# Kernel optimization log

Hardware: AMD Instinct MI355X
Metric: run time of the kernel (lower is better)

The kernel has to match this reference:

```python
import jax, jax.numpy as jnp
import numpy as np

KERNEL = 2
STRIDE = 2
N_QUBITS = 4
N_LAYERS = 2
PI = np.float32(np.pi)
EPS = np.float32(1e-8)


def setup_inputs() -> dict:
    key = jax.random.key(0)
    k1, k2, k3, k4 = jax.random.split(key, 4)
    x = jax.random.normal(k1, (64, 3, 512, 512), dtype=jnp.float32)
    weights = jax.random.normal(k2, (N_LAYERS, N_QUBITS, 3), dtype=jnp.float32) * 0.1
    proj_w = jax.random.normal(k3, (4, N_QUBITS, 1, 1), dtype=jnp.float32) * 0.5
    proj_b = jax.random.normal(k4, (4,), dtype=jnp.float32) * 0.1
    return {"x": x, "weights": weights, "proj_w": proj_w, "proj_b": proj_b}


def _extract_patches(x):
    # x: (B, C, H, W) -> flattened 2x2 patches of grayscale image: (B, Ho, Wo, 4)
    B, C, H, W = x.shape
    Ho = (H - KERNEL) // STRIDE + 1
    Wo = (W - KERNEL) // STRIDE + 1
    x_gray = x.mean(axis=1)  # (B, H, W)
    # stride == kernel, so non-overlapping patches via reshape
    p = x_gray.reshape(B, Ho, KERNEL, Wo, KERNEL)
    p = p.transpose(0, 1, 3, 2, 4).reshape(B, Ho, Wo, KERNEL * KERNEL)
    return p


def reference(x, weights, proj_w, proj_b):
    patches = _extract_patches(x)  # (B, Ho, Wo, 4)
    # global min-max normalization (matches patches.min()/max() over whole tensor)
    pmin = patches.min()
    pmax = patches.max()
    patches = (patches - pmin) / (pmax - pmin + EPS)

    # simplified quantum simulation, fully vectorized over (B, Ho, Wo)
    encoded = jnp.sin(patches * PI)  # (B, Ho, Wo, Q)
    for layer in range(N_LAYERS):
        w = weights[layer]  # (Q, 3)
        neighbor = jnp.roll(encoded, shift=-1, axis=-1)  # encoded[(i+1)%Q]
        mixed = encoded * jnp.cos(w[:, 0]) + neighbor * jnp.sin(w[:, 1]) + w[:, 2]
        encoded = jnp.tanh(mixed)

    # (B, Ho, Wo, Q) -> (B, Q, Ho, Wo), then 1x1 conv projection
    q = encoded.transpose(0, 3, 1, 2)
    out = jnp.einsum('bqhw,oq->bohw', q, proj_w[:, :, 0, 0]) + proj_b[None, :, None, None]
    return out
```

## Files before the change

### kernel.cpp

```cpp
#include <hip/hip_runtime.h>
#include <hip/hip_fp16.h>

constexpr int BN = 64, CH = 3, HH = 512, WW = 512;
constexpr int HO = 256, WO = 256;
constexpr int HW = HH * WW;
constexpr int HOWO = HO * WO;
constexpr float EPS_F = 1e-8f;

constexpr int TPB = 256;
constexpr int GROUPS = BN * HO * (WO / 4);
constexpr int ABLOCKS = 2048;
constexpr int AT = ABLOCKS * TPB;
constexpr int AITERS = GROUPS / AT;
constexpr int CBLOCKS = GROUPS / TPB;

constexpr size_t GRAY_HALFS = (size_t)GROUPS * 16;

__device__ __forceinline__ float fast_tanh(float x) {
    float t = __builtin_amdgcn_exp2f(x * 2.8853900817779268f);
    return 1.0f - 2.0f * __builtin_amdgcn_rcpf(t + 1.0f);
}

__global__ __launch_bounds__(TPB) void k_pass1(const float* __restrict__ x,
                                               float4* __restrict__ gray4,
                                               float* __restrict__ part) {
    const int tid = blockIdx.x * TPB + threadIdx.x;
    const float c13 = 1.0f / 3.0f;
    float vmin = __int_as_float(0x7F800000);
    float vmax = __int_as_float(0xFF800000);

    #pragma unroll
    for (int it = 0; it < AITERS; ++it) {
        int grp = it * AT + tid;
        int b   = grp >> 14;
        int rem = grp & 16383;
        int ho  = rem >> 6;
        int wp  = rem & 63;
        const float* base = x + b * (CH * HW) + (2 * ho) * WW + 8 * wp;

        float row0[8], row1[8];
        #pragma unroll
        for (int c = 0; c < CH; ++c) {
            const float* pc = base + c * HW;
            float4 u0 = *(const float4*)(pc);
            float4 u1 = *(const float4*)(pc + 4);
            float4 v0 = *(const float4*)(pc + WW);
            float4 v1 = *(const float4*)(pc + WW + 4);
            float uu[8] = {u0.x, u0.y, u0.z, u0.w, u1.x, u1.y, u1.z, u1.w};
            float vv[8] = {v0.x, v0.y, v0.z, v0.w, v1.x, v1.y, v1.z, v1.w};
            if (c == 0) {
                #pragma unroll
                for (int k = 0; k < 8; ++k) { row0[k] = uu[k]; row1[k] = vv[k]; }
            } else {
                #pragma unroll
                for (int k = 0; k < 8; ++k) { row0[k] += uu[k]; row1[k] += vv[k]; }
            }
        }
        #pragma unroll
        for (int k = 0; k < 8; ++k) {
            row0[k] *= c13; row1[k] *= c13;
            vmin = fminf(vmin, fminf(row0[k], row1[k]));
            vmax = fmaxf(vmax, fmaxf(row0[k], row1[k]));
        }
        alignas(16) __half2 h2[8];
        #pragma unroll
        for (int p = 0; p < 4; ++p) {
            h2[2 * p]     = __floats2half2_rn(row0[2 * p], row0[2 * p + 1]);
            h2[2 * p + 1] = __floats2half2_rn(row1[2 * p], row1[2 * p + 1]);
        }
        gray4[(size_t)grp * 2]     = *(const float4*)&h2[0];
        gray4[(size_t)grp * 2 + 1] = *(const float4*)&h2[4];
    }

    #pragma unroll
    for (int off = 32; off > 0; off >>= 1) {
        vmin = fminf(vmin, __shfl_down(vmin, off, 64));
        vmax = fmaxf(vmax, __shfl_down(vmax, off, 64));
    }
    __shared__ float sm[8];
    int lane = threadIdx.x & 63, wid = threadIdx.x >> 6;
    if (lane == 0) { sm[wid] = vmin; sm[4 + wid] = vmax; }
    __syncthreads();
    if (threadIdx.x == 0) {
        part[2 * blockIdx.x]     = fminf(fminf(sm[0], sm[1]), fminf(sm[2], sm[3]));
        part[2 * blockIdx.x + 1] = fmaxf(fmaxf(sm[4], sm[5]), fmaxf(sm[6], sm[7]));
    }
}

__global__ __launch_bounds__(TPB) void k_reduce(const float* __restrict__ part,
                                                float* __restrict__ mm) {
    float m = __int_as_float(0x7F800000);
    float M = __int_as_float(0xFF800000);
    #pragma unroll
    for (int i = 0; i < ABLOCKS / TPB; ++i) {
        int j = i * TPB + threadIdx.x;
        m = fminf(m, part[2 * j]);
        M = fmaxf(M, part[2 * j + 1]);
    }
    #pragma unroll
    for (int off = 32; off > 0; off >>= 1) {
        m = fminf(m, __shfl_down(m, off, 64));
        M = fmaxf(M, __shfl_down(M, off, 64));
    }
    __shared__ float sm[8];
    int lane = threadIdx.x & 63, wid = threadIdx.x >> 6;
    if (lane == 0) { sm[wid] = m; sm[4 + wid] = M; }
    __syncthreads();
    if (threadIdx.x == 0) {
        mm[0] = fminf(fminf(sm[0], sm[1]), fminf(sm[2], sm[3]));
        mm[1] = fmaxf(fmaxf(sm[4], sm[5]), fmaxf(sm[6], sm[7]));
    }
}

__global__ __launch_bounds__(TPB) void k_main(const float4* __restrict__ gray4,
                                              const float* __restrict__ wts,
                                              const float* __restrict__ pw,
                                              const float* __restrict__ pb,
                                              const float* __restrict__ mm,
                                              float* __restrict__ out) {
    int grp = blockIdx.x * TPB + threadIdx.x;
    int b   = grp >> 14;
    int rem = grp & 16383;
    int ho  = rem >> 6;
    int wp  = rem & 63;

    float pmin   = mm[0];
    float sscale = 0.5f / (mm[1] - pmin + EPS_F);

    const float inv2pi = 0.15915494309189535f;
    float c0[2][4], s1[2][4], b2[2][4];
    #pragma unroll
    for (int l = 0; l < 2; ++l)
        #pragma unroll
        for (int q = 0; q < 4; ++q) {
            c0[l][q] = __builtin_amdgcn_cosf(wts[(l * 4 + q) * 3 + 0] * inv2pi);
            s1[l][q] = __builtin_amdgcn_sinf(wts[(l * 4 + q) * 3 + 1] * inv2pi);
            b2[l][q] = wts[(l * 4 + q) * 3 + 2];
        }
    float pwr[4][4], pbr[4];
    #pragma unroll
    for (int o = 0; o < 4; ++o) {
        pbr[o] = pb[o];
        #pragma unroll
        for (int q = 0; q < 4; ++q) pwr[o][q] = pw[o * 4 + q];
    }

    alignas(16) __half2 h2[8];
    *(float4*)&h2[0] = gray4[(size_t)grp * 2];
    *(float4*)&h2[4] = gray4[(size_t)grp * 2 + 1];

    float e[4][4];
    #pragma unroll
    for (int p = 0; p < 4; ++p) {
        e[p][0] = __low2float(h2[2 * p]);     e[p][1] = __high2float(h2[2 * p]);
        e[p][2] = __low2float(h2[2 * p + 1]); e[p][3] = __high2float(h2[2 * p + 1]);
    }
    #pragma unroll
    for (int p = 0; p < 4; ++p)
        #pragma unroll
        for (int q = 0; q < 4; ++q)
            e[p][q] = __builtin_amdgcn_sinf((e[p][q] - pmin) * sscale);
    #pragma unroll
    for (int l = 0; l < 2; ++l)
        #pragma unroll
        for (int p = 0; p < 4; ++p) {
            float mq[4];
            #pragma unroll
            for (int q = 0; q < 4; ++q)
                mq[q] = e[p][q] * c0[l][q] + e[p][(q + 1) & 3] * s1[l][q] + b2[l][q];
            #pragma unroll
            for (int q = 0; q < 4; ++q) e[p][q] = fast_tanh(mq[q]);
        }

    float* ob = out + b * (4 * HOWO) + ho * WO + 4 * wp;
    #pragma unroll
    for (int o = 0; o < 4; ++o) {
        float4 v;
        float* vp = &v.x;
        #pragma unroll
        for (int p = 0; p < 4; ++p) {
            float acc = pbr[o];
            #pragma unroll
            for (int q = 0; q < 4; ++q) acc += e[p][q] * pwr[o][q];
            vp[p] = acc;
        }
        *(float4*)(ob + o * HOWO) = v;
    }
}

extern "C" void kernel_launch(void* const* d_in, const int* in_sizes, int n_in,
                              void* d_out, int out_size, void* d_ws, size_t ws_size,
                              hipStream_t stream) {
    const float* x   = (const float*)d_in[0];
    const float* wts = (const float*)d_in[1];
    const float* pw  = (const float*)d_in[2];
    const float* pb  = (const float*)d_in[3];
    float* out = (float*)d_out;

    float4* gray4 = (float4*)d_ws;
    float*  part  = (float*)((char*)d_ws + GRAY_HALFS * sizeof(__half));
    float*  mm    = part + 2 * ABLOCKS;

    k_pass1 <<<ABLOCKS, TPB, 0, stream>>>(x, gray4, part);
    k_reduce<<<1,       TPB, 0, stream>>>(part, mm);
    k_main  <<<CBLOCKS, TPB, 0, stream>>>(gray4, wts, pw, pb, mm, out);
}
```

Before: 314.1 us.

## Fuse three kernels into one persistent kernel with grid-wide barrier for min/max

Replaces the gray-write, reduce and main kernels with a single persistent kernel of 1024 blocks. Each thread keeps its half-precision gray patches in registers, publishes block min/max, and spins on an atomic counter as a grid barrier. Every block then reduces all partials itself and computes outputs from the values it holds. This removes the round trip of the gray intermediate through global memory and two launches, at the cost of a memset, a spin barrier that needs all 1024 blocks resident at once (launch bounds ask for 4 per CU), and higher register pressure.

```diff
diff --git a/kernel.cpp b/kernel.cpp
--- a/kernel.cpp
+++ b/kernel.cpp
@@ -7,31 +7,34 @@
 constexpr int HOWO = HO * WO;
 constexpr float EPS_F = 1e-8f;
 
-constexpr int TPB = 256;
+constexpr int BLOCKS = 1024, TPB = 256;
+constexpr int T = BLOCKS * TPB;
 constexpr int GROUPS = BN * HO * (WO / 4);
-constexpr int ABLOCKS = 2048;
-constexpr int AT = ABLOCKS * TPB;
-constexpr int AITERS = GROUPS / AT;
-constexpr int CBLOCKS = GROUPS / TPB;
-
-constexpr size_t GRAY_HALFS = (size_t)GROUPS * 16;
+constexpr int ITERS = GROUPS / T;
+
+constexpr int PART_OFF = 64;
 
 __device__ __forceinline__ float fast_tanh(float x) {
     float t = __builtin_amdgcn_exp2f(x * 2.8853900817779268f);
     return 1.0f - 2.0f * __builtin_amdgcn_rcpf(t + 1.0f);
 }
 
-__global__ __launch_bounds__(TPB) void k_pass1(const float* __restrict__ x,
-                                               float4* __restrict__ gray4,
-                                               float* __restrict__ part) {
+__global__ __launch_bounds__(TPB, 4) void k_fused(
+    const float* __restrict__ x, const float* __restrict__ wts,
+    const float* __restrict__ pw, const float* __restrict__ pb,
+    unsigned int* __restrict__ cnt, float* __restrict__ part,
+    float* __restrict__ out)
+{
     const int tid = blockIdx.x * TPB + threadIdx.x;
     const float c13 = 1.0f / 3.0f;
+
+    __half2 g[ITERS][8];
     float vmin = __int_as_float(0x7F800000);
     float vmax = __int_as_float(0xFF800000);
 
     #pragma unroll
-    for (int it = 0; it < AITERS; ++it) {
-        int grp = it * AT + tid;
+    for (int it = 0; it < ITERS; ++it) {
+        int grp = it * T + tid;
         int b   = grp >> 14;
         int rem = grp & 16383;
         int ho  = rem >> 6;
@@ -62,14 +65,11 @@
             vmin = fminf(vmin, fminf(row0[k], row1[k]));
             vmax = fmaxf(vmax, fmaxf(row0[k], row1[k]));
         }
-        alignas(16) __half2 h2[8];
         #pragma unroll
         for (int p = 0; p < 4; ++p) {
-            h2[2 * p]     = __floats2half2_rn(row0[2 * p], row0[2 * p + 1]);
-            h2[2 * p + 1] = __floats2half2_rn(row1[2 * p], row1[2 * p + 1]);
-        }
-        gray4[(size_t)grp * 2]     = *(const float4*)&h2[0];
-        gray4[(size_t)grp * 2 + 1] = *(const float4*)&h2[4];
+            g[it][2 * p]     = __floats2half2_rn(row0[2 * p], row0[2 * p + 1]);
+            g[it][2 * p + 1] = __floats2half2_rn(row1[2 * p], row1[2 * p + 1]);
+        }
     }
 
     #pragma unroll
@@ -78,54 +78,45 @@
         vmax = fmaxf(vmax, __shfl_down(vmax, off, 64));
     }
     __shared__ float sm[8];
+    __shared__ float sfin[2];
     int lane = threadIdx.x & 63, wid = threadIdx.x >> 6;
     if (lane == 0) { sm[wid] = vmin; sm[4 + wid] = vmax; }
     __syncthreads();
+
     if (threadIdx.x == 0) {
-        part[2 * blockIdx.x]     = fminf(fminf(sm[0], sm[1]), fminf(sm[2], sm[3]));
-        part[2 * blockIdx.x + 1] = fmaxf(fmaxf(sm[4], sm[5]), fmaxf(sm[6], sm[7]));
-    }
-}
-
-__global__ __launch_bounds__(TPB) void k_reduce(const float* __restrict__ part,
-                                                float* __restrict__ mm) {
+        float m = fminf(fminf(sm[0], sm[1]), fminf(sm[2], sm[3]));
+        float M = fmaxf(fmaxf(sm[4], sm[5]), fmaxf(sm[6], sm[7]));
+        __hip_atomic_store(&part[2 * blockIdx.x],     m, __ATOMIC_RELAXED, __HIP_MEMORY_SCOPE_AGENT);
+        __hip_atomic_store(&part[2 * blockIdx.x + 1], M, __ATOMIC_RELAXED, __HIP_MEMORY_SCOPE_AGENT);
+        __hip_atomic_fetch_add(cnt, 1u, __ATOMIC_RELEASE, __HIP_MEMORY_SCOPE_AGENT);
+        while (__hip_atomic_load(cnt, __ATOMIC_ACQUIRE, __HIP_MEMORY_SCOPE_AGENT) < (unsigned)BLOCKS)
+            __builtin_amdgcn_s_sleep(2);
+    }
+    __syncthreads();
+
     float m = __int_as_float(0x7F800000);
     float M = __int_as_float(0xFF800000);
     #pragma unroll
-    for (int i = 0; i < ABLOCKS / TPB; ++i) {
+    for (int i = 0; i < BLOCKS / TPB; ++i) {
         int j = i * TPB + threadIdx.x;
-        m = fminf(m, part[2 * j]);
-        M = fmaxf(M, part[2 * j + 1]);
+        m = fminf(m, __hip_atomic_load(&part[2 * j],     __ATOMIC_RELAXED, __HIP_MEMORY_SCOPE_AGENT));
+        M = fmaxf(M, __hip_atomic_load(&part[2 * j + 1], __ATOMIC_RELAXED, __HIP_MEMORY_SCOPE_AGENT));
     }
     #pragma unroll
     for (int off = 32; off > 0; off >>= 1) {
         m = fminf(m, __shfl_down(m, off, 64));
         M = fmaxf(M, __shfl_down(M, off, 64));
     }
-    __shared__ float sm[8];
-    int lane = threadIdx.x & 63, wid = threadIdx.x >> 6;
     if (lane == 0) { sm[wid] = m; sm[4 + wid] = M; }
     __syncthreads();
     if (threadIdx.x == 0) {
-        mm[0] = fminf(fminf(sm[0], sm[1]), fminf(sm[2], sm[3]));
-        mm[1] = fmaxf(fmaxf(sm[4], sm[5]), fmaxf(sm[6], sm[7]));
-    }
-}
-
-__global__ __launch_bounds__(TPB) void k_main(const float4* __restrict__ gray4,
-                                              const float* __restrict__ wts,
-                                              const float* __restrict__ pw,
-                                              const float* __restrict__ pb,
-                                              const float* __restrict__ mm,
-                                              float* __restrict__ out) {
-    int grp = blockIdx.x * TPB + threadIdx.x;
-    int b   = grp >> 14;
-    int rem = grp & 16383;
-    int ho  = rem >> 6;
-    int wp  = rem & 63;
-
-    float pmin   = mm[0];
-    float sscale = 0.5f / (mm[1] - pmin + EPS_F);
+        sfin[0] = fminf(fminf(sm[0], sm[1]), fminf(sm[2], sm[3]));
+        sfin[1] = fmaxf(fmaxf(sm[4], sm[5]), fmaxf(sm[6], sm[7]));
+    }
+    __syncthreads();
+
+    float pmin   = sfin[0];
+    float sscale = 0.5f / (sfin[1] - pmin + EPS_F);
 
     const float inv2pi = 0.15915494309189535f;
     float c0[2][4], s1[2][4], b2[2][4];
@@ -145,46 +136,52 @@
         for (int q = 0; q < 4; ++q) pwr[o][q] = pw[o * 4 + q];
     }
 
-    alignas(16) __half2 h2[8];
-    *(float4*)&h2[0] = gray4[(size_t)grp * 2];
-    *(float4*)&h2[4] = gray4[(size_t)grp * 2 + 1];
-
-    float e[4][4];
-    #pragma unroll
-    for (int p = 0; p < 4; ++p) {
-        e[p][0] = __low2float(h2[2 * p]);     e[p][1] = __high2float(h2[2 * p]);
-        e[p][2] = __low2float(h2[2 * p + 1]); e[p][3] = __high2float(h2[2 * p + 1]);
-    }
-    #pragma unroll
-    for (int p = 0; p < 4; ++p)
-        #pragma unroll
-        for (int q = 0; q < 4; ++q)
-            e[p][q] = __builtin_amdgcn_sinf((e[p][q] - pmin) * sscale);
-    #pragma unroll
-    for (int l = 0; l < 2; ++l)
+    #pragma unroll
+    for (int it = 0; it < ITERS; ++it) {
+        int grp = it * T + tid;
+        int b   = grp >> 14;
+        int rem = grp & 16383;
+        int ho  = rem >> 6;
+        int wp  = rem & 63;
+
+        float e[4][4];
         #pragma unroll
         for (int p = 0; p < 4; ++p) {
-            float mq[4];
+            __half2 h0 = g[it][2 * p], h1 = g[it][2 * p + 1];
+            e[p][0] = __low2float(h0);  e[p][1] = __high2float(h0);
+            e[p][2] = __low2float(h1);  e[p][3] = __high2float(h1);
+        }
+        #pragma unroll
+        for (int p = 0; p < 4; ++p)
             #pragma unroll
             for (int q = 0; q < 4; ++q)
-                mq[q] = e[p][q] * c0[l][q] + e[p][(q + 1) & 3] * s1[l][q] + b2[l][q];
+                e[p][q] = __builtin_amdgcn_sinf((e[p][q] - pmin) * sscale);
+        #pragma unroll
+        for (int l = 0; l < 2; ++l)
             #pragma unroll
-            for (int q = 0; q < 4; ++q) e[p][q] = fast_tanh(mq[q]);
-        }
-
-    float* ob = out + b * (4 * HOWO) + ho * WO + 4 * wp;
-    #pragma unroll
-    for (int o = 0; o < 4; ++o) {
-        float4 v;
-        float* vp = &v.x;
-        #pragma unroll
-        for (int p = 0; p < 4; ++p) {
-            float acc = pbr[o];
+            for (int p = 0; p < 4; ++p) {
+                float mq[4];
+                #pragma unroll
+                for (int q = 0; q < 4; ++q)
+                    mq[q] = e[p][q] * c0[l][q] + e[p][(q + 1) & 3] * s1[l][q] + b2[l][q];
+                #pragma unroll
+                for (int q = 0; q < 4; ++q) e[p][q] = fast_tanh(mq[q]);
+            }
+
+        float* ob = out + b * (4 * HOWO) + ho * WO + 4 * wp;
+        #pragma unroll
+        for (int o = 0; o < 4; ++o) {
+            float4 v;
+            float* vp = &v.x;
             #pragma unroll
-            for (int q = 0; q < 4; ++q) acc += e[p][q] * pwr[o][q];
-            vp[p] = acc;
-        }
-        *(float4*)(ob + o * HOWO) = v;
+            for (int p = 0; p < 4; ++p) {
+                float acc = pbr[o];
+                #pragma unroll
+                for (int q = 0; q < 4; ++q) acc += e[p][q] * pwr[o][q];
+                vp[p] = acc;
+            }
+            *(float4*)(ob + o * HOWO) = v;
+        }
     }
 }
 
@@ -197,11 +194,9 @@
     const float* pb  = (const float*)d_in[3];
     float* out = (float*)d_out;
 
-    float4* gray4 = (float4*)d_ws;
-    float*  part  = (float*)((char*)d_ws + GRAY_HALFS * sizeof(__half));
-    float*  mm    = part + 2 * ABLOCKS;
-
-    k_pass1 <<<ABLOCKS, TPB, 0, stream>>>(x, gray4, part);
-    k_reduce<<<1,       TPB, 0, stream>>>(part, mm);
-    k_main  <<<CBLOCKS, TPB, 0, stream>>>(gray4, wts, pw, pb, mm, out);
+    unsigned int* cnt = (unsigned int*)d_ws;
+    float* part = (float*)d_ws + PART_OFF;
+
+    hipMemsetAsync(d_ws, 0, sizeof(unsigned int), stream);
+    k_fused<<<BLOCKS, TPB, 0, stream>>>(x, wts, pw, pb, cnt, part, out);
 }
```

After: 476.9 us. +51.8%, slower.
